# Performance work log

Hardware: AMD Instinct MI355X
Metric: run time of the kernel (lower is better)

The kernel has to match this reference:

```python
import jax, jax.numpy as jnp
import numpy as np

TAU = [1, 2, 4, 8]
B, T, FC, FX = 128, 2048, 512, 512


def setup_inputs() -> dict:
    key = jax.random.key(0)
    k1, k2, k3, k4 = jax.random.split(key, 4)
    C = jax.random.normal(k1, (B, T, FC), dtype=jnp.float32)
    X = jax.random.normal(k2, (B, T, FX), dtype=jnp.float32)
    # one Linear(encoding_size -> context_size) per tau; torch weight layout [out, in]
    W = jax.random.normal(k3, (len(TAU), FC, FX), dtype=jnp.float32) * (1.0 / np.sqrt(FX))
    b = jax.random.normal(k4, (len(TAU), FC), dtype=jnp.float32) * 0.01
    return {"C": C, "X": X, "W": W, "b": b}


def _infonce(Ct, Xe, Wk, bk):
    # Ct: [B, Tt, fc], Xe: [B, Tt, fx]
    Xt = jnp.einsum('btf,gf->btg', Xe, Wk) + bk          # Linear: [B, Tt, fc]
    Z = jnp.einsum('itf,jtf->ijt', Ct, Xt)               # scores [B, B, Tt]
    Zmax = jnp.max(Z, axis=1, keepdims=True)             # [B, 1, Tt]
    lse = jnp.log(jnp.sum(jnp.exp(Z - Zmax), axis=1)) + Zmax[:, 0]  # [B, Tt]
    Zdiag = jnp.diagonal(Z, axis1=0, axis2=1).T          # Z[i,i,t] -> [B, Tt]
    return jnp.mean(Zdiag - lse)


def reference(C, X, W, b):
    losses = [_infonce(C[:, :-t], X[:, t:], W[k], b[k]) for k, t in enumerate(TAU)]
    return jnp.stack(losses)
```

## Files before the change

kernel.cpp:

```cpp
#include <hip/hip_runtime.h>
#include <math.h>

constexpr int Tn  = 2048;
constexpr int FCn = 512;
constexpr int FXn = 512;
constexpr int SXW = 72;
constexpr int SYC = 136;
constexpr int SZS = 132;

typedef __attribute__((ext_vector_type(8))) short  bf16x8;
typedef __attribute__((ext_vector_type(4))) float  f32x4;

__device__ __forceinline__ unsigned pk2(float a, float b) {
  return __builtin_amdgcn_perm(__float_as_uint(b), __float_as_uint(a), 0x07060302u);
}
__device__ __forceinline__ uint4 pack8(float4 a, float4 b) {
  uint4 rv;
  rv.x = pk2(a.x, a.y); rv.y = pk2(a.z, a.w);
  rv.z = pk2(b.x, b.y); rv.w = pk2(b.z, b.w);
  return rv;
}

__device__ __forceinline__ void gll16(const unsigned short* g, void* lds) {
  __builtin_amdgcn_global_load_lds(
      (const __attribute__((address_space(1))) unsigned int*)g,
      (__attribute__((address_space(3))) unsigned int*)lds, 16, 0, 0);
}

__global__ void zero4(float* out) {
  if (threadIdx.x < 4) out[threadIdx.x] = 0.0f;
}

__global__ void finalize4(float* out) {
  int k = threadIdx.x;
  if (k < 4) out[k] *= 1.0f / (128.0f * (float)(Tn - (1 << k)));
}

__global__ void tobf16(const float* __restrict__ s, unsigned short* __restrict__ d) {
  int i = blockIdx.x * 256 + threadIdx.x;
  float4 v = ((const float4*)s)[i];
  uint2 p; p.x = pk2(v.x, v.y); p.y = pk2(v.z, v.w);
  ((uint2*)d)[i] = p;
}

__global__ __launch_bounds__(256, 2)
void infonce_v7(const float* __restrict__ Cp, const unsigned short* __restrict__ Xb,
                const unsigned short* __restrict__ Wb, float* __restrict__ out)
{
  __shared__ __align__(16) unsigned char smem[67648];
  char* sm   = (char*)smem;
  char* sWc  = sm + 16384;
  float* sZ  = (float*)sm;
  float* sRed = (float*)(sm + 67584);

  const int tid  = threadIdx.x;
  const int lane = tid & 63;
  const int wave = tid >> 6;
  const int r    = lane & 15;
  const int h    = lane >> 4;
  const int jw   = wave >> 1;
  const int gw   = wave & 1;
  const int iw   = wave >> 1;
  const int jw2  = wave & 1;

  const int orig = blockIdx.x;
  const int xcd  = orig & 7;
  const int loc  = orig >> 3;
  const int wg   = (xcd < 4) ? (xcd * 1024 + loc) : (4096 + (xcd - 4) * 1023 + loc);
  const int k    = wg & 3;
  const int t    = wg >> 2;
  const int tau  = 1 << k;
  if (t >= Tn - tau) return;
  const int s = t + tau;

  const int colg = (lane & 7) ^ (lane >> 3);
  const unsigned short* xlane = Xb + (size_t)(wave * 32 + (lane >> 3)) * (Tn * FXn)
                                + (size_t)s * FXn + colg * 8;
  const unsigned short* wlane = Wb + (size_t)k * (FCn * FXn)
                                + (size_t)(wave * 64 + (lane >> 3)) * FXn + colg * 8;
  char* xdst = sm  + wave * 4096;
  char* wdst = sWc + wave * 8192;

  const float* cr0 = Cp + (size_t)(iw * 64 +  0 + r) * (Tn * FCn) + (size_t)t * FCn;
  const float* cr1 = Cp + (size_t)(iw * 64 + 16 + r) * (Tn * FCn) + (size_t)t * FCn;
  const float* cr2 = Cp + (size_t)(iw * 64 + 32 + r) * (Tn * FCn) + (size_t)t * FCn;
  const float* cr3 = Cp + (size_t)(iw * 64 + 48 + r) * (Tn * FCn) + (size_t)t * FCn;

  f32x4 zacc[4][4];
#pragma unroll
  for (int a = 0; a < 4; ++a)
#pragma unroll
    for (int b = 0; b < 4; ++b) zacc[a][b] = f32x4{0.f, 0.f, 0.f, 0.f};

#pragma unroll 1
  for (int gc = 0; gc < 2; ++gc) {
    f32x4 yacc[4][8];
#pragma unroll
    for (int a = 0; a < 4; ++a)
#pragma unroll
      for (int b = 0; b < 8; ++b) yacc[a][b] = f32x4{0.f, 0.f, 0.f, 0.f};

#pragma unroll 1
    for (int xc = 0; xc < 8; ++xc) {
      __syncthreads();
#pragma unroll
      for (int i = 0; i < 4; ++i)
        gll16(xlane + (size_t)(i * 8) * (Tn * FXn) + xc * 64, xdst + i * 1024);
#pragma unroll
      for (int i = 0; i < 8; ++i)
        gll16(wlane + (size_t)(gc * 256 + i * 8) * FXn + xc * 64, wdst + i * 1024);
      __syncthreads();
#pragma unroll
      for (int ks = 0; ks < 2; ++ks) {
        const int cbx = (ks * 64 + h * 16) ^ ((r & 7) << 4);
        bf16x8 ax[4], bw[8];
#pragma unroll
        for (int bm = 0; bm < 4; ++bm)
          ax[bm] = *(const bf16x8*)(sm + (jw * 64 + bm * 16 + r) * 128 + cbx);
#pragma unroll
        for (int bn = 0; bn < 8; ++bn)
          bw[bn] = *(const bf16x8*)(sWc + (gw * 128 + bn * 16 + r) * 128 + cbx);
        __builtin_amdgcn_s_setprio(1);
#pragma unroll
        for (int bm = 0; bm < 4; ++bm)
#pragma unroll
          for (int bn = 0; bn < 8; ++bn)
            yacc[bm][bn] = __builtin_amdgcn_mfma_f32_16x16x32_bf16(
                ax[bm], bw[bn], yacc[bm][bn], 0, 0, 0);
        __builtin_amdgcn_s_setprio(0);
      }
    }
    __syncthreads();
#pragma unroll
    for (int bm = 0; bm < 4; ++bm)
#pragma unroll
      for (int bn = 0; bn < 8; ++bn)
#pragma unroll
        for (int reg = 0; reg < 4; ++reg) {
          const int row = jw * 64 + bm * 16 + h * 4 + reg;
          const int col = gw * 128 + bn * 16 + r;
          *(unsigned short*)(sm + row * 528 + col * 2) =
              (unsigned short)(__float_as_uint(yacc[bm][bn][reg]) >> 16);
        }
    __syncthreads();
#pragma unroll 2
    for (int ks2 = 0; ks2 < 8; ++ks2) {
      const int goff = gc * 256 + ks2 * 32 + h * 8;
      const int gb   = ks2 * 64 + h * 16;
      bf16x8 ac[4], by[4];
      {
        float4 u0 = *(const float4*)(cr0 + goff);
        float4 v0 = *(const float4*)(cr0 + goff + 4);
        float4 u1 = *(const float4*)(cr1 + goff);
        float4 v1 = *(const float4*)(cr1 + goff + 4);
        float4 u2 = *(const float4*)(cr2 + goff);
        float4 v2 = *(const float4*)(cr2 + goff + 4);
        float4 u3 = *(const float4*)(cr3 + goff);
        float4 v3 = *(const float4*)(cr3 + goff + 4);
        ac[0] = __builtin_bit_cast(bf16x8, pack8(u0, v0));
        ac[1] = __builtin_bit_cast(bf16x8, pack8(u1, v1));
        ac[2] = __builtin_bit_cast(bf16x8, pack8(u2, v2));
        ac[3] = __builtin_bit_cast(bf16x8, pack8(u3, v3));
      }
#pragma unroll
      for (int bn = 0; bn < 4; ++bn)
        by[bn] = *(const bf16x8*)(sm + (jw2 * 64 + bn * 16 + r) * 528 + gb);
      __builtin_amdgcn_s_setprio(1);
#pragma unroll
      for (int bm = 0; bm < 4; ++bm)
#pragma unroll
        for (int bn = 0; bn < 4; ++bn)
          zacc[bm][bn] = __builtin_amdgcn_mfma_f32_16x16x32_bf16(
              ac[bm], by[bn], zacc[bm][bn], 0, 0, 0);
      __builtin_amdgcn_s_setprio(0);
    }
  }
  __syncthreads();
#pragma unroll
  for (int bm = 0; bm < 4; ++bm)
#pragma unroll
    for (int bn = 0; bn < 4; ++bn)
#pragma unroll
      for (int reg = 0; reg < 4; ++reg)
        sZ[(iw * 64 + bm * 16 + h * 4 + reg) * SZS + (jw2 * 64 + bn * 16 + r)] =
            zacc[bm][bn][reg];
  __syncthreads();

  const int row = wave * 32 + (lane >> 1);
  const int c0l = lane & 1;
  float mx = -3.4e38f;
#pragma unroll
  for (int m = 0; m < 64; ++m) mx = fmaxf(mx, sZ[row * SZS + c0l + m * 2]);
  mx = fmaxf(mx, __shfl_xor(mx, 1));
  float sum = 0.f;
#pragma unroll
  for (int m = 0; m < 64; ++m) sum += __expf(sZ[row * SZS + c0l + m * 2] - mx);
  sum += __shfl_xor(sum, 1);
  float val = (c0l == 0) ? (sZ[row * SZS + row] - (__logf(sum) + mx)) : 0.f;
#pragma unroll
  for (int off = 1; off < 64; off <<= 1) val += __shfl_xor(val, off);
  if (lane == 0) sRed[wave] = val;
  __syncthreads();
  if (tid == 0) atomicAdd(out + k, sRed[0] + sRed[1] + sRed[2] + sRed[3]);
}

template <bool WBF>
__global__ __launch_bounds__(512, 4)
void infonce_main(const float* __restrict__ Cp, const float* __restrict__ Xp,
                  const void* __restrict__ Wp, float* __restrict__ out)
{
  __shared__ __align__(16) unsigned char smem[71680];
  unsigned short* sX = (unsigned short*)(smem);
  unsigned short* sW = (unsigned short*)(smem + 18432);
  unsigned short* sY = (unsigned short*)(smem + 36864);
  unsigned short* sC = (unsigned short*)(smem);
  float* sZ   = (float*)(smem);
  float* sRed = (float*)(smem + 67584);

  const int tid  = threadIdx.x;
  const int lane = tid & 63;
  const int wave = tid >> 6;
  const int r    = lane & 15;
  const int h    = lane >> 4;
  const int wr   = wave >> 1;
  const int wc   = wave & 1;

  const int orig = blockIdx.x;
  const int xcd  = orig & 7;
  const int loc  = orig >> 3;
  const int wg   = (xcd < 4) ? (xcd * 1024 + loc) : (4096 + (xcd - 4) * 1023 + loc);
  const int k    = wg & 3;
  const int t    = wg >> 2;
  const int tau  = 1 << k;
  if (t >= Tn - tau) return;

  const float* Cb = Cp + (size_t)t * FCn;
  const float* Xb = Xp + (size_t)(t + tau) * FXn;

  const int srow = tid >> 2;
  const int scol = (tid & 3) * 16;
  const float* xs = Xb + (size_t)srow * (Tn * FXn) + scol;
  unsigned short* xd = sX + srow * SXW + scol;
  unsigned short* wd = sW + srow * SXW + scol;
  const unsigned short* wsh = (const unsigned short*)Wp + (size_t)k * (FCn * FXn)
                              + (size_t)srow * FXn + scol;
  const float* wsf = (const float*)Wp + (size_t)k * (FCn * FXn)
                     + (size_t)srow * FXn + scol;
  const int crow0 = tid >> 4;
  const int ccol  = (tid & 15) * 8;
  const float* cs = Cb + (size_t)crow0 * (Tn * FCn) + ccol;
  unsigned short* cd = sC + crow0 * SYC + ccol;
  const size_t cstep = (size_t)32 * Tn * FCn;

  float4 px0, px1, px2, px3;
  float4 pw0, pw1, pw2, pw3;
  uint4  pb0, pb1;
  float4 pc0, pc1, pc2, pc3, pc4, pc5, pc6, pc7;

#define LOAD_X(XC) do { \
    const float4* _p = (const float4*)(xs + (XC) * 64); \
    px0 = _p[0]; px1 = _p[1]; px2 = _p[2]; px3 = _p[3]; } while (0)
#define LOAD_W(GC, XC) do { \
    if constexpr (WBF) { \
      const uint4* _p = (const uint4*)(wsh + (size_t)((GC) * 128) * FXn + (XC) * 64); \
      pb0 = _p[0]; pb1 = _p[1]; \
    } else { \
      const float4* _p = (const float4*)(wsf + (size_t)((GC) * 128) * FXn + (XC) * 64); \
      pw0 = _p[0]; pw1 = _p[1]; pw2 = _p[2]; pw3 = _p[3]; } } while (0)
#define STORE_XW() do { \
    *(uint4*)(xd)     = pack8(px0, px1); \
    *(uint4*)(xd + 8) = pack8(px2, px3); \
    if constexpr (WBF) { *(uint4*)(wd) = pb0; *(uint4*)(wd + 8) = pb1; } \
    else { *(uint4*)(wd) = pack8(pw0, pw1); *(uint4*)(wd + 8) = pack8(pw2, pw3); } \
  } while (0)
#define MFMA_YF() do { \
    _Pragma("unroll") \
    for (int ks = 0; ks < 2; ++ks) { \
      const int xoo = ks * 32 + h * 8; \
      bf16x8 a0 = *(const bf16x8*)(sX + (wr * 32 + 0  + r) * SXW + xoo); \
      bf16x8 a1 = *(const bf16x8*)(sX + (wr * 32 + 16 + r) * SXW + xoo); \
      _Pragma("unroll") \
      for (int bg = 0; bg < 4; ++bg) { \
        bf16x8 bb = *(const bf16x8*)(sW + (wc * 64 + bg * 16 + r) * SXW + xoo); \
        yacc[0][bg] = __builtin_amdgcn_mfma_f32_16x16x32_bf16(a0, bb, yacc[0][bg], 0, 0, 0); \
        yacc[1][bg] = __builtin_amdgcn_mfma_f32_16x16x32_bf16(a1, bb, yacc[1][bg], 0, 0, 0); \
      } } } while (0)

  f32x4 zacc[2][4];
#pragma unroll
  for (int a = 0; a < 2; ++a)
#pragma unroll
    for (int b = 0; b < 4; ++b) zacc[a][b] = f32x4{0.f, 0.f, 0.f, 0.f};

  LOAD_X(0); LOAD_W(0, 0);

  for (int gc = 0; gc < 4; ++gc) {
    f32x4 yacc[2][4];
#pragma unroll
    for (int a = 0; a < 2; ++a)
#pragma unroll
      for (int b = 0; b < 4; ++b) yacc[a][b] = f32x4{0.f, 0.f, 0.f, 0.f};

    for (int xc = 0; xc < 7; ++xc) {
      __syncthreads();
      STORE_XW();
      __syncthreads();
      LOAD_X(xc + 1); LOAD_W(gc, xc + 1);
      MFMA_YF();
    }
    __syncthreads();
    STORE_XW();
    __syncthreads();
    {
      const float4* p0 = (const float4*)(cs + 0 * cstep + gc * 128);
      const float4* p1 = (const float4*)(cs + 1 * cstep + gc * 128);
      const float4* p2 = (const float4*)(cs + 2 * cstep + gc * 128);
      const float4* p3 = (const float4*)(cs + 3 * cstep + gc * 128);
      pc0 = p0[0]; pc1 = p0[1];
      pc2 = p1[0]; pc3 = p1[1];
      pc4 = p2[0]; pc5 = p2[1];
      pc6 = p3[0]; pc7 = p3[1];
    }
    MFMA_YF();

#pragma unroll
    for (int aj = 0; aj < 2; ++aj)
#pragma unroll
      for (int bg = 0; bg < 4; ++bg)
#pragma unroll
        for (int reg = 0; reg < 4; ++reg)
          sY[(wr * 32 + aj * 16 + h * 4 + reg) * SYC + (wc * 64 + bg * 16 + r)] =
              (unsigned short)(__float_as_uint(yacc[aj][bg][reg]) >> 16);
    __syncthreads();
    *(uint4*)(cd + 0 * 32 * SYC) = pack8(pc0, pc1);
    *(uint4*)(cd + 1 * 32 * SYC) = pack8(pc2, pc3);
    *(uint4*)(cd + 2 * 32 * SYC) = pack8(pc4, pc5);
    *(uint4*)(cd + 3 * 32 * SYC) = pack8(pc6, pc7);
    __syncthreads();
    if (gc < 3) { LOAD_X(0); LOAD_W(gc + 1, 0); }
#pragma unroll
    for (int ks = 0; ks < 4; ++ks) {
      const int go = ks * 32 + h * 8;
      bf16x8 a0 = *(const bf16x8*)(sC + (wr * 32 + 0  + r) * SYC + go);
      bf16x8 a1 = *(const bf16x8*)(sC + (wr * 32 + 16 + r) * SYC + go);
#pragma unroll
      for (int bj = 0; bj < 4; ++bj) {
        bf16x8 bb = *(const bf16x8*)(sY + (wc * 64 + bj * 16 + r) * SYC + go);
        zacc[0][bj] = __builtin_amdgcn_mfma_f32_16x16x32_bf16(a0, bb, zacc[0][bj], 0, 0, 0);
        zacc[1][bj] = __builtin_amdgcn_mfma_f32_16x16x32_bf16(a1, bb, zacc[1][bj], 0, 0, 0);
      }
    }
  }
  __syncthreads();
#pragma unroll
  for (int ai = 0; ai < 2; ++ai)
#pragma unroll
    for (int bj = 0; bj < 4; ++bj)
#pragma unroll
      for (int reg = 0; reg < 4; ++reg)
        sZ[(wr * 32 + ai * 16 + h * 4 + reg) * SZS + (wc * 64 + bj * 16 + r)] =
            zacc[ai][bj][reg];
  __syncthreads();

  const int row = wave * 16 + (lane >> 2);
  const int c0l = lane & 3;
  float mx = -3.4e38f;
#pragma unroll
  for (int m = 0; m < 32; ++m) mx = fmaxf(mx, sZ[row * SZS + c0l + m * 4]);
  mx = fmaxf(mx, __shfl_xor(mx, 1));
  mx = fmaxf(mx, __shfl_xor(mx, 2));
  float sum = 0.f;
#pragma unroll
  for (int m = 0; m < 32; ++m) sum += __expf(sZ[row * SZS + c0l + m * 4] - mx);
  sum += __shfl_xor(sum, 1);
  sum += __shfl_xor(sum, 2);
  float val = (c0l == 0) ? (sZ[row * SZS + row] - (__logf(sum) + mx)) : 0.f;
#pragma unroll
  for (int off = 1; off < 64; off <<= 1) val += __shfl_xor(val, off);
  if (lane == 0) sRed[wave] = val;
  __syncthreads();
  if (tid == 0) {
    float bs = 0.f;
#pragma unroll
    for (int w2 = 0; w2 < 8; ++w2) bs += sRed[w2];
    atomicAdd(out + k, bs);
  }
#undef LOAD_X
#undef LOAD_W
#undef STORE_XW
#undef MFMA_YF
}

extern "C" void kernel_launch(void* const* d_in, const int* in_sizes, int n_in,
                              void* d_out, int out_size, void* d_ws, size_t ws_size,
                              hipStream_t stream) {
  const float* C = (const float*)d_in[0];
  const float* X = (const float*)d_in[1];
  const float* W = (const float*)d_in[2];
  float* out = (float*)d_out;

  const size_t NX = (size_t)128 * Tn * FXn;
  const size_t NW = (size_t)4 * FCn * FXn;
  const size_t WS_W   = NW * 2;
  const size_t WS_MID = WS_W + NX * 2;

  hipLaunchKernelGGL(zero4, dim3(1), dim3(64), 0, stream, out);

  if (ws_size >= WS_MID) {
    unsigned short* Wbf = (unsigned short*)d_ws;
    unsigned short* Xbf = (unsigned short*)((char*)d_ws + WS_W);
    hipLaunchKernelGGL(tobf16, dim3((unsigned)(NW / 1024)), dim3(256), 0, stream, W, Wbf);
    hipLaunchKernelGGL(tobf16, dim3((unsigned)(NX / 1024)), dim3(256), 0, stream, X, Xbf);
    hipLaunchKernelGGL(infonce_v7, dim3(2047 * 4), dim3(256), 0, stream,
                       C, Xbf, Wbf, out);
  } else if (ws_size >= WS_W) {
    hipLaunchKernelGGL(tobf16, dim3((unsigned)(NW / 1024)), dim3(256), 0, stream,
                       W, (unsigned short*)d_ws);
    hipLaunchKernelGGL(infonce_main<true>, dim3(2047 * 4), dim3(512), 0, stream,
                       C, X, (const void*)d_ws, out);
  } else {
    hipLaunchKernelGGL(infonce_main<false>, dim3(2047 * 4), dim3(512), 0, stream,
                       C, X, (const void*)W, out);
  }
  hipLaunchKernelGGL(finalize4, dim3(1), dim3(64), 0, stream, out);
}
```

Baseline: 1.392 ms.

## Shrink LDS footprint by staging Y and Z tiles in halves

Y (the projected X tile) is now written to shared memory in two 128-column halves. The second GEMM runs over each half in turn, so the Y buffer only needs 128 columns. The score matrix is likewise written and reduced one 64-row half at a time, which cuts shared memory from about 66KB to 48KB. This is meant to allow more resident workgroups per CU. It adds extra barriers and serialises the store and compute phases. The s_setprio hints are also removed.

```diff
diff --git a/kernel.cpp b/kernel.cpp
--- a/kernel.cpp
+++ b/kernel.cpp
@@ -44,14 +44,15 @@
 }
 
 __global__ __launch_bounds__(256, 2)
-void infonce_v7(const float* __restrict__ Cp, const unsigned short* __restrict__ Xb,
-                const unsigned short* __restrict__ Wb, float* __restrict__ out)
+void infonce_v15(const float* __restrict__ Cp, const unsigned short* __restrict__ Xb,
+                 const unsigned short* __restrict__ Wb, float* __restrict__ out)
 {
-  __shared__ __align__(16) unsigned char smem[67648];
+  __shared__ __align__(16) unsigned char smem[49168];
   char* sm   = (char*)smem;
   char* sWc  = sm + 16384;
-  float* sZ  = (float*)sm;
-  float* sRed = (float*)(sm + 67584);
+  unsigned short* sY = (unsigned short*)sm;
+  float* sZh  = (float*)sm;
+  float* sRed = (float*)(sm + 49152);
 
   const int tid  = threadIdx.x;
   const int lane = tid & 63;
@@ -120,83 +121,95 @@
 #pragma unroll
         for (int bn = 0; bn < 8; ++bn)
           bw[bn] = *(const bf16x8*)(sWc + (gw * 128 + bn * 16 + r) * 128 + cbx);
-        __builtin_amdgcn_s_setprio(1);
 #pragma unroll
         for (int bm = 0; bm < 4; ++bm)
 #pragma unroll
           for (int bn = 0; bn < 8; ++bn)
             yacc[bm][bn] = __builtin_amdgcn_mfma_f32_16x16x32_bf16(
                 ax[bm], bw[bn], yacc[bm][bn], 0, 0, 0);
-        __builtin_amdgcn_s_setprio(0);
       }
     }
     __syncthreads();
-#pragma unroll
-    for (int bm = 0; bm < 4; ++bm)
-#pragma unroll
-      for (int bn = 0; bn < 8; ++bn)
-#pragma unroll
-        for (int reg = 0; reg < 4; ++reg) {
-          const int row = jw * 64 + bm * 16 + h * 4 + reg;
-          const int col = gw * 128 + bn * 16 + r;
-          *(unsigned short*)(sm + row * 528 + col * 2) =
-              (unsigned short)(__float_as_uint(yacc[bm][bn][reg]) >> 16);
+
+#pragma unroll 1
+    for (int hz = 0; hz < 2; ++hz) {
+      if (gw == hz) {
+#pragma unroll
+        for (int bm = 0; bm < 4; ++bm)
+#pragma unroll
+          for (int bn = 0; bn < 8; ++bn)
+#pragma unroll
+            for (int reg = 0; reg < 4; ++reg) {
+              const int row = jw * 64 + bm * 16 + h * 4 + reg;
+              const int col = bn * 16 + r;
+              sY[row * SYC + col] =
+                  (unsigned short)(__float_as_uint(yacc[bm][bn][reg]) >> 16);
+            }
+      }
+      __syncthreads();
+#pragma unroll
+      for (int ks2 = 0; ks2 < 4; ++ks2) {
+        const int goff = gc * 256 + hz * 128 + ks2 * 32 + h * 8;
+        const int yo   = ks2 * 32 + h * 8;
+        bf16x8 ac[4], by[4];
+        {
+          float4 u0 = *(const float4*)(cr0 + goff);
+          float4 v0 = *(const float4*)(cr0 + goff + 4);
+          float4 u1 = *(const float4*)(cr1 + goff);
+          float4 v1 = *(const float4*)(cr1 + goff + 4);
+          float4 u2 = *(const float4*)(cr2 + goff);
+          float4 v2 = *(const float4*)(cr2 + goff + 4);
+          float4 u3 = *(const float4*)(cr3 + goff);
+          float4 v3 = *(const float4*)(cr3 + goff + 4);
+          ac[0] = __builtin_bit_cast(bf16x8, pack8(u0, v0));
+          ac[1] = __builtin_bit_cast(bf16x8, pack8(u1, v1));
+          ac[2] = __builtin_bit_cast(bf16x8, pack8(u2, v2));
+          ac[3] = __builtin_bit_cast(bf16x8, pack8(u3, v3));
         }
-    __syncthreads();
-#pragma unroll 2
-    for (int ks2 = 0; ks2 < 8; ++ks2) {
-      const int goff = gc * 256 + ks2 * 32 + h * 8;
-      const int gb   = ks2 * 64 + h * 16;
-      bf16x8 ac[4], by[4];
-      {
-        float4 u0 = *(const float4*)(cr0 + goff);
-        float4 v0 = *(const float4*)(cr0 + goff + 4);
-        float4 u1 = *(const float4*)(cr1 + goff);
-        float4 v1 = *(const float4*)(cr1 + goff + 4);
-        float4 u2 = *(const float4*)(cr2 + goff);
-        float4 v2 = *(const float4*)(cr2 + goff + 4);
-        float4 u3 = *(const float4*)(cr3 + goff);
-        float4 v3 = *(const float4*)(cr3 + goff + 4);
-        ac[0] = __builtin_bit_cast(bf16x8, pack8(u0, v0));
-        ac[1] = __builtin_bit_cast(bf16x8, pack8(u1, v1));
-        ac[2] = __builtin_bit_cast(bf16x8, pack8(u2, v2));
-        ac[3] = __builtin_bit_cast(bf16x8, pack8(u3, v3));
+#pragma unroll
+        for (int bn = 0; bn < 4; ++bn)
+          by[bn] = *(const bf16x8*)(sY + (jw2 * 64 + bn * 16 + r) * SYC + yo);
+#pragma unroll
+        for (int bm = 0; bm < 4; ++bm)
+#pragma unroll
+          for (int bn = 0; bn < 4; ++bn)
+            zacc[bm][bn] = __builtin_amdgcn_mfma_f32_16x16x32_bf16(
+                ac[bm], by[bn], zacc[bm][bn], 0, 0, 0);
       }
-#pragma unroll
-      for (int bn = 0; bn < 4; ++bn)
-        by[bn] = *(const bf16x8*)(sm + (jw2 * 64 + bn * 16 + r) * 528 + gb);
-      __builtin_amdgcn_s_setprio(1);
+      __syncthreads();
+    }
+  }
+
+  float val = 0.f;
+#pragma unroll 1
+  for (int p = 0; p < 2; ++p) {
+    if (iw == p) {
 #pragma unroll
       for (int bm = 0; bm < 4; ++bm)
 #pragma unroll
         for (int bn = 0; bn < 4; ++bn)
-          zacc[bm][bn] = __builtin_amdgcn_mfma_f32_16x16x32_bf16(
-              ac[bm], by[bn], zacc[bm][bn], 0, 0, 0);
-      __builtin_amdgcn_s_setprio(0);
-    }
+#pragma unroll
+          for (int reg = 0; reg < 4; ++reg)
+            sZh[(bm * 16 + h * 4 + reg) * SZS + (jw2 * 64 + bn * 16 + r)] =
+                zacc[bm][bn][reg];
+    }
+    __syncthreads();
+    const int row = wave * 16 + (lane >> 2);
+    const int c0l = lane & 3;
+    float mx = -3.4e38f;
+#pragma unroll
+    for (int m = 0; m < 32; ++m) mx = fmaxf(mx, sZh[row * SZS + c0l + m * 4]);
+    mx = fmaxf(mx, __shfl_xor(mx, 1));
+    mx = fmaxf(mx, __shfl_xor(mx, 2));
+    float sum = 0.f;
+#pragma unroll
+    for (int m = 0; m < 32; ++m) sum += __expf(sZh[row * SZS + c0l + m * 4] - mx);
+    sum += __shfl_xor(sum, 1);
+    sum += __shfl_xor(sum, 2);
+    if (c0l == 0)
+      val += sZh[row * SZS + (p * 64 + row)] - (__logf(sum) + mx);
+    __syncthreads();
   }
-  __syncthreads();
-#pragma unroll
-  for (int bm = 0; bm < 4; ++bm)
-#pragma unroll
-    for (int bn = 0; bn < 4; ++bn)
-#pragma unroll
-      for (int reg = 0; reg < 4; ++reg)
-        sZ[(iw * 64 + bm * 16 + h * 4 + reg) * SZS + (jw2 * 64 + bn * 16 + r)] =
-            zacc[bm][bn][reg];
-  __syncthreads();
-
-  const int row = wave * 32 + (lane >> 1);
-  const int c0l = lane & 1;
-  float mx = -3.4e38f;
-#pragma unroll
-  for (int m = 0; m < 64; ++m) mx = fmaxf(mx, sZ[row * SZS + c0l + m * 2]);
-  mx = fmaxf(mx, __shfl_xor(mx, 1));
-  float sum = 0.f;
-#pragma unroll
-  for (int m = 0; m < 64; ++m) sum += __expf(sZ[row * SZS + c0l + m * 2] - mx);
-  sum += __shfl_xor(sum, 1);
-  float val = (c0l == 0) ? (sZ[row * SZS + row] - (__logf(sum) + mx)) : 0.f;
 #pragma unroll
   for (int off = 1; off < 64; off <<= 1) val += __shfl_xor(val, off);
   if (lane == 0) sRed[wave] = val;
@@ -411,7 +424,7 @@
     unsigned short* Xbf = (unsigned short*)((char*)d_ws + WS_W);
     hipLaunchKernelGGL(tobf16, dim3((unsigned)(NW / 1024)), dim3(256), 0, stream, W, Wbf);
     hipLaunchKernelGGL(tobf16, dim3((unsigned)(NX / 1024)), dim3(256), 0, stream, X, Xbf);
-    hipLaunchKernelGGL(infonce_v7, dim3(2047 * 4), dim3(256), 0, stream,
+    hipLaunchKernelGGL(infonce_v15, dim3(2047 * 4), dim3(256), 0, stream,
                        C, Xbf, Wbf, out);
   } else if (ws_size >= WS_W) {
     hipLaunchKernelGGL(tobf16, dim3((unsigned)(NW / 1024)), dim3(256), 0, stream,
```

New measurement: 2.001 ms. +43.7%, slower.
